# Kernel tuning notes

Measured on AMD Instinct MI355X. Metric: run time of the kernel, lower is better.

Reference implementation:

```python
import jax, jax.numpy as jnp
import numpy as np

N = 256        # SSM state size
D_MODEL = 2048 # number of independent channels sharing the kernel
L_MAX = 4096   # sequence length


def setup_inputs() -> dict:
    key = jax.random.key(0)
    k1, k2, k3, k4 = jax.random.split(key, 4)
    s = float(np.sqrt(N))
    # Stable A: eigenvalues with negative real part so A^l stays bounded after
    # bilinear discretization with step = 1/L.
    A = 0.5 * jax.random.normal(k1, (N, N), jnp.float32) / s - jnp.eye(N, dtype=jnp.float32)
    B = jax.random.normal(k2, (N, 1), jnp.float32) / s   # lecun-scale
    C = jax.random.normal(k3, (1, N), jnp.float32) / s
    D = jnp.ones((1,), jnp.float32)
    y = jax.random.normal(k4, (D_MODEL, L_MAX), jnp.float32)
    return {"y": y, "A": A, "B": B, "C": C, "D": D}


def _build_kernel(A, B, C, L, step):
    # Bilinear (Tustin) discretization, as in discretize_SSM.
    I = jnp.eye(A.shape[0], dtype=A.dtype)
    BL = jnp.linalg.inv(I - (step / 2.0) * A)
    Abar = BL @ (I + (step / 2.0) * A)
    Bbar = (BL * step) @ B                      # (N, 1)
    # K[l] = C @ Abar^l @ Bbar, computed as L matvecs via scan
    # (same math as the matrix_power loop, without O(L*N^3) cost).
    def step_fn(x, _):
        return Abar @ x, (C @ x)[0]
    _, K = jax.lax.scan(step_fn, Bbar[:, 0], None, length=L)
    return K                                     # (L,)


def _causal_conv(y, K):
    # mode='full' convolution truncated to first L samples == causal conv.
    L = y.shape[-1]
    n = 2 * L
    Yf = jnp.fft.rfft(y, n=n, axis=-1)           # (d_model, n//2+1)
    Kf = jnp.fft.rfft(K, n=n)                    # (n//2+1,)
    return jnp.fft.irfft(Yf * Kf, n=n, axis=-1)[..., :L]


def reference(y, A, B, C, D):
    L = y.shape[-1]
    K = _build_kernel(A, B, C, L, step=1.0 / L)
    return _causal_conv(y, K) + D * y
```

## Files before the change

kernel.cpp:

```cpp
#include <hip/hip_runtime.h>

#define N_ 256
#define L_ 4096
#define DM_ 2048
#define STEPF (1.0f / 4096.0f)
#define NW 15
#define NV 6
#define RQN 4608

typedef short bf16x8 __attribute__((ext_vector_type(8)));
typedef float f32x4 __attribute__((ext_vector_type(4)));
typedef unsigned int uint32;

__device__ __forceinline__ uint32 bf16rne(float f) {
    uint32 u = __builtin_bit_cast(uint32, f);
    return (u + 0x7FFFu + ((u >> 16) & 1u)) >> 16;
}
__device__ __forceinline__ float rdlane(float v, int l) {
    return __builtin_bit_cast(float, __builtin_amdgcn_readlane(__builtin_bit_cast(int, v), l));
}

__global__ __launch_bounds__(1024) void k_kry(const float* __restrict__ Araw,
                                              const float* __restrict__ Bv,
                                              const float* __restrict__ Cv,
                                              float* __restrict__ W,
                                              float* __restrict__ V) {
    __shared__ float kry[NW][256];
    __shared__ float red[4][256];
    __shared__ float cur[256];
    const int tid = threadIdx.x;
    const int j = tid & 255, seg = tid >> 8, lane = tid & 63;

#define DOT64(S0, S1, VV) { \
    _Pragma("unroll") \
    for (int m = 0; m < 64; m += 2) { \
        S0 = fmaf(rdlane(VV, m), a[m], S0); \
        S1 = fmaf(rdlane(VV, m + 1), a[m + 1], S1); \
    } }

    if (blockIdx.x == 0) {
        float a[64];
#pragma unroll
        for (int m = 0; m < 64; ++m) a[m] = Araw[(64 * seg + m) * 256 + j];
        if (tid < 256) kry[0][tid] = Cv[tid];
        __syncthreads();
        const float WSC = 4032.0f / 4096.0f;
        for (int n = 1; n < NW; ++n) {
            float vv = kry[n - 1][64 * seg + lane];
            float s0 = 0.f, s1 = 0.f;
            DOT64(s0, s1, vv)
            red[seg][j] = s0 + s1;
            __syncthreads();
            if (tid < 256)
                kry[n][tid] = (red[0][tid] + red[1][tid] + red[2][tid] + red[3][tid]) * (WSC / (float)n);
            __syncthreads();
        }
        float kj[NW];
#pragma unroll
        for (int n = 0; n < NW; ++n) kj[n] = kry[n][j];
        for (int u = 0; u < 16; ++u) {
            int q = seg + 4 * u;
            float c = (float)q * (1.0f / 63.0f);
            float h = kj[NW - 1];
#pragma unroll
            for (int n = NW - 2; n >= 0; --n) h = fmaf(c, h, kj[n]);
            W[q * 256 + j] = h;
        }
    } else {
        float a[64];
#pragma unroll
        for (int m = 0; m < 64; ++m) a[m] = Araw[j * 256 + 64 * seg + m];
        if (tid < 256) cur[tid] = Bv[tid];
        __syncthreads();
        const float ms = 0.5f * STEPF;
        for (int it = 0; it < 3; ++it) {
            float vv = cur[64 * seg + lane];
            float s0 = 0.f, s1 = 0.f;
            DOT64(s0, s1, vv)
            red[seg][j] = s0 + s1;
            __syncthreads();
            if (tid < 256)
                cur[tid] = fmaf(ms, red[0][tid] + red[1][tid] + red[2][tid] + red[3][tid], Bv[tid]);
            __syncthreads();
        }
        if (tid < 256) kry[0][tid] = STEPF * cur[tid];
        __syncthreads();
        const float VSC = 63.0f / 4096.0f;
        for (int n = 1; n < NV; ++n) {
            float vv = kry[n - 1][64 * seg + lane];
            float s0 = 0.f, s1 = 0.f;
            DOT64(s0, s1, vv)
            red[seg][j] = s0 + s1;
            __syncthreads();
            if (tid < 256)
                kry[n][tid] = (red[0][tid] + red[1][tid] + red[2][tid] + red[3][tid]) * (VSC / (float)n);
            __syncthreads();
        }
        float kj[NV];
#pragma unroll
        for (int n = 0; n < NV; ++n) kj[n] = kry[n][j];
        for (int u = 0; u < 16; ++u) {
            int r = seg + 4 * u;
            float c = (float)r * (1.0f / 63.0f);
            float h = kj[NV - 1];
#pragma unroll
            for (int n = NV - 2; n >= 0; --n) h = fmaf(c, h, kj[n]);
            V[j * 64 + r] = h;
        }
    }
#undef DOT64
}

__global__ __launch_bounds__(256) void k_g(const float* __restrict__ A, const float* __restrict__ B,
                                           float* __restrict__ C, int Ma, int Nb,
                                           int lda, int ldb, int ldc, float alpha, float diagv) {
    int row0 = blockIdx.y * 32, col0 = blockIdx.x * 32;
    if (row0 >= Ma || col0 >= Nb) return;
    __shared__ float As[16][33], Bs[16][33];
    int tid = threadIdx.x;
    int tx = tid & 15, ty = tid >> 4;
    int e0 = tid * 2, e1 = e0 + 1;
    int ai0 = e0 >> 4, ak0 = e0 & 15, ai1 = e1 >> 4, ak1 = e1 & 15;
    int bj0 = e0 & 31, bk0 = e0 >> 5, bj1 = e1 & 31, bk1 = e1 >> 5;
    bool va0 = (row0 + ai0) < Ma, va1 = (row0 + ai1) < Ma;
    bool vb0 = (col0 + bj0) < Nb, vb1 = (col0 + bj1) < Nb;
    float a0p = va0 ? A[(row0 + ai0) * lda + ak0] : 0.f;
    float a1p = va1 ? A[(row0 + ai1) * lda + ak1] : 0.f;
    float b0p = vb0 ? B[bk0 * ldb + col0 + bj0] : 0.f;
    float b1p = vb1 ? B[bk1 * ldb + col0 + bj1] : 0.f;
    float acc00 = 0.f, acc01 = 0.f, acc10 = 0.f, acc11 = 0.f;
    for (int kk = 0; kk < 256; kk += 16) {
        As[ak0][ai0] = a0p; As[ak1][ai1] = a1p;
        Bs[bk0][bj0] = b0p; Bs[bk1][bj1] = b1p;
        __syncthreads();
        if (kk + 16 < 256) {
            a0p = va0 ? A[(row0 + ai0) * lda + kk + 16 + ak0] : 0.f;
            a1p = va1 ? A[(row0 + ai1) * lda + kk + 16 + ak1] : 0.f;
            b0p = vb0 ? B[(bk0 + kk + 16) * ldb + col0 + bj0] : 0.f;
            b1p = vb1 ? B[(bk1 + kk + 16) * ldb + col0 + bj1] : 0.f;
        }
#pragma unroll
        for (int k = 0; k < 16; ++k) {
            float a0 = As[k][ty * 2], a1 = As[k][ty * 2 + 1];
            float b0 = Bs[k][tx * 2], b1 = Bs[k][tx * 2 + 1];
            acc00 = fmaf(a0, b0, acc00); acc01 = fmaf(a0, b1, acc01);
            acc10 = fmaf(a1, b0, acc10); acc11 = fmaf(a1, b1, acc11);
        }
        __syncthreads();
    }
    float accs[2][2] = {{acc00, acc01}, {acc10, acc11}};
#pragma unroll
    for (int i = 0; i < 2; ++i) {
        int r = row0 + ty * 2 + i;
        if (r < Ma)
#pragma unroll
            for (int jj = 0; jj < 2; ++jj) {
                int c = col0 + tx * 2 + jj;
                if (c < Nb) {
                    float v = alpha * accs[i][jj];
                    if (r == c) v += diagv;
                    C[r * ldc + c] = v;
                }
            }
    }
}

__global__ __launch_bounds__(256) void k_pack(const float* __restrict__ Kf, uint2* __restrict__ Rqg) {
    int i = blockIdx.x * 256 + threadIdx.x;
    int a = 4095 - i;
    uint32 e0 = (a >= 0) ? bf16rne(Kf[a]) : 0u;
    uint32 e1 = (a >= 1) ? bf16rne(Kf[a - 1]) : 0u;
    uint32 e2 = (a >= 2) ? bf16rne(Kf[a - 2]) : 0u;
    uint32 e3 = (a >= 3) ? bf16rne(Kf[a - 3]) : 0u;
    uint2 v; v.x = e0 | (e1 << 16); v.y = e2 | (e3 << 16);
    Rqg[i] = v;
}

__global__ __launch_bounds__(256, 2) void k_conv(const uint2* __restrict__ Rqg,
                                                 const float* __restrict__ y,
                                                 const float* __restrict__ Dp,
                                                 float* __restrict__ out) {
    __shared__ uint2 Rq[RQN];
    __shared__ f32x4 mbuf[2][8][64];
    const int tid = threadIdx.x;
#pragma unroll
    for (int i = 0; i < RQN / 256; ++i) Rq[i * 256 + tid] = Rqg[i * 256 + tid];
    __syncthreads();

    const int w = tid >> 6, lane = tid & 63;
    const int n = lane & 15, g = lane >> 4;
    const int ds = w & 1, jh = w >> 1;
    const int by = (int)blockIdx.y;
    const int d0w = (int)blockIdx.x * 32 + ds * 16;
    const int d = d0w + n;
    const float4* __restrict__ yq = (const float4*)(y + (size_t)d * L_);
    const float D0 = Dp[0];

#define LOADF(SL, I0) { \
    uint2 u0 = Rq[(I0)]; uint2 u1 = Rq[(I0) + 4]; \
    uint4 uu; uu.x = u0.x; uu.y = u0.y; uu.z = u1.x; uu.w = u1.y; \
    fr[SL] = __builtin_bit_cast(bf16x8, uu); }
#define PK2(LO, HI) __builtin_amdgcn_perm(__builtin_bit_cast(uint32, (HI)), \
                                          __builtin_bit_cast(uint32, (LO)), 0x07060302u)
#define PACKAV(Q0, Q1) { \
    uint4 ua; ua.x = PK2((Q0).x, (Q0).y); ua.y = PK2((Q0).z, (Q0).w); \
    ua.z = PK2((Q1).x, (Q1).y); ua.w = PK2((Q1).z, (Q1).w); \
    av = __builtin_bit_cast(bf16x8, ua); }
#define MF(TI, SL) acc[TI] = __builtin_amdgcn_mfma_f32_16x16x32_bf16(av, fr[SL], acc[TI], 0, 0, 0);

#define STEPB(YI, S0,S1,S2,S3,S4,S5,S6,S7,S8,S9,S10,S11,S12,S13,S14,S15) { \
    PACKAV(q0a, q0b); \
    q0a = q1a; q0b = q1b; \
    __builtin_amdgcn_s_setprio(1); \
    MF(14, S14) MF(15, S15) \
    LOADF(S14, bcur + 32) LOADF(S15, bcur + 16) \
    q1a = yq[(YI)]; q1b = yq[(YI) + 1]; \
    yn += 8; bcur += 32; \
    MF(0,S0) MF(1,S1) MF(2,S2) MF(3,S3) MF(4,S4) MF(5,S5) MF(6,S6) MF(7,S7) \
    MF(8,S8) MF(9,S9) MF(10,S10) MF(11,S11) MF(12,S12) MF(13,S13) \
    __builtin_amdgcn_s_setprio(0); \
}

#define ROUND8(YIM) \
    STEPB(YIM, 0,1,2,3,4,5,6,7,8,9,10,11,12,13,14,15) \
    STEPB(YIM, 14,15,0,1,2,3,4,5,6,7,8,9,10,11,12,13) \
    STEPB(YIM, 12,13,14,15,0,1,2,3,4,5,6,7,8,9,10,11) \
    STEPB(YIM, 10,11,12,13,14,15,0,1,2,3,4,5,6,7,8,9) \
    STEPB(YIM, 8,9,10,11,12,13,14,15,0,1,2,3,4,5,6,7) \
    STEPB(YIM, 6,7,8,9,10,11,12,13,14,15,0,1,2,3,4,5) \
    STEPB(YIM, 4,5,6,7,8,9,10,11,12,13,14,15,0,1,2,3) \
    STEPB(YIM, 2,3,4,5,6,7,8,9,10,11,12,13,14,15,0,1)

#define ROUND4(YIM) \
    STEPB(YIM, 0,1,2,3,4,5,6,7,8,9,10,11,12,13,14,15) \
    STEPB(YIM, 14,15,0,1,2,3,4,5,6,7,8,9,10,11,12,13) \
    STEPB(YIM, 12,13,14,15,0,1,2,3,4,5,6,7,8,9,10,11) \
    STEPB(YIM, 10,11,12,13,14,15,0,1,2,3,4,5,6,7,8,9)

    for (int strip = 0; strip < 2; ++strip) {
        const int v = strip ? by : (15 - by);
        const int t0 = v << 8;
        const int Sh = 4 * (v + 1);
        const int s0 = jh * Sh;

        f32x4 acc[16];
#pragma unroll
        for (int i = 0; i < 16; ++i) acc[i] = (f32x4){0.f, 0.f, 0.f, 0.f};
        bf16x8 fr[16], av;
        float4 q0a, q0b, q1a, q1b;

        const int B0 = 4095 - t0 - n + 8 * g + 32 * s0;
#pragma unroll
        for (int ti = 0; ti < 16; ++ti) LOADF(ti, B0 - 16 * ti)
        q0a = yq[8 * s0 + 2 * g];     q0b = yq[8 * s0 + 2 * g + 1];
        q1a = yq[8 * s0 + 8 + 2 * g]; q1b = yq[8 * s0 + 8 + 2 * g + 1];
        int bcur = B0;
        int yn = 8 * s0 + 16 + 2 * g;

        const int n8 = Sh >> 3;
        for (int it = 0; it < n8 - 1; ++it) {
            ROUND8(yn)
        }
        if (n8 > 0) {
            ROUND8(yn < 1016 ? yn : 1016)
        }
        if (Sh & 4) {
            ROUND4(yn)
        }

#pragma unroll
        for (int rr = 0; rr < 2; ++rr) {
            if (jh == 1) {
#pragma unroll
                for (int i = 0; i < 8; ++i) mbuf[ds][i][lane] = acc[rr * 8 + i];
            }
            __syncthreads();
            if (jh == 0) {
#pragma unroll
                for (int i = 0; i < 8; ++i) {
                    f32x4 m = mbuf[ds][i][lane];
                    acc[rr * 8 + i][0] += m[0]; acc[rr * 8 + i][1] += m[1];
                    acc[rr * 8 + i][2] += m[2]; acc[rr * 8 + i][3] += m[3];
                }
            }
            __syncthreads();
        }
        if (jh == 0) {
#pragma unroll
            for (int ti = 0; ti < 16; ++ti) {
                int tcol = t0 + 16 * ti + n;
#pragma unroll
                for (int r = 0; r < 4; ++r) {
                    int dr = d0w + 4 * g + r;
                    size_t ix = (size_t)dr * L_ + tcol;
                    out[ix] = acc[ti][r] + D0 * y[ix];
                }
            }
        }
    }

#undef ROUND8
#undef ROUND4
#undef STEPB
#undef MF
#undef PACKAV
#undef PK2
#undef LOADF
}


extern "C" void kernel_launch(void* const* d_in, const int* in_sizes, int n_in,
                              void* d_out, int out_size, void* d_ws, size_t ws_size,
                              hipStream_t stream) {
    const float* y  = (const float*)d_in[0];
    const float* A  = (const float*)d_in[1];
    const float* Bv = (const float*)d_in[2];
    const float* Cv = (const float*)d_in[3];
    const float* Dp = (const float*)d_in[4];
    float* out = (float*)d_out;
    float* w = (float*)d_ws;

    float* W   = w;
    float* V   = w + 16384;
    float* Kf  = w + 32768;
    uint2* Rqg = (uint2*)(w + 36864);

    k_kry<<<dim3(2), dim3(1024), 0, stream>>>(A, Bv, Cv, W, V);
    k_g<<<dim3(2, 2), dim3(256), 0, stream>>>(W, V, Kf, 64, 64, 256, 64, 64, 1.0f, 0.0f);
    k_pack<<<dim3(18), dim3(256), 0, stream>>>(Kf, Rqg);
    k_conv<<<dim3(64, 8), dim3(256), 0, stream>>>(Rqg, y, Dp, out);

    (void)in_sizes; (void)n_in; (void)out_size; (void)ws_size;
}
```

Before: 80.27 us.

## Fuse Krylov build, small GEMM and bf16 pack into one kernel

Merges the two-block Krylov kernel, the 64x64 GEMM kernel and the bf16 pack kernel into a single one-block kernel that keeps W, V and Kf in shared memory. This removes two kernel launches and the global round trips for the intermediates. In exchange, the W and V Krylov chains that previously ran in parallel on two blocks now run serially in one block, and about 148KB of shared memory is used.

```diff
diff --git a/kernel.cpp b/kernel.cpp
--- a/kernel.cpp
+++ b/kernel.cpp
@@ -20,16 +20,21 @@
     return __builtin_bit_cast(float, __builtin_amdgcn_readlane(__builtin_bit_cast(int, v), l));
 }
 
-__global__ __launch_bounds__(1024) void k_kry(const float* __restrict__ Araw,
-                                              const float* __restrict__ Bv,
-                                              const float* __restrict__ Cv,
-                                              float* __restrict__ W,
-                                              float* __restrict__ V) {
-    __shared__ float kry[NW][256];
-    __shared__ float red[4][256];
-    __shared__ float cur[256];
+__global__ __launch_bounds__(1024) void k_build(const float* __restrict__ Araw,
+                                                const float* __restrict__ Bv,
+                                                const float* __restrict__ Cv,
+                                                uint2* __restrict__ Rqg) {
+    __shared__ float sm[37888];
+    float* kry = sm;
+    float* red = sm + 3840;
+    float* cur = sm + 4864;
+    float* Wl  = sm + 5120;
+    float* Vl  = sm + 21504;
+    float* Kf  = sm;
+
     const int tid = threadIdx.x;
     const int j = tid & 255, seg = tid >> 8, lane = tid & 63;
+    float a[64];
 
 #define DOT64(S0, S1, VV) { \
     _Pragma("unroll") \
@@ -38,142 +43,116 @@
         S1 = fmaf(rdlane(VV, m + 1), a[m + 1], S1); \
     } }
 
-    if (blockIdx.x == 0) {
-        float a[64];
-#pragma unroll
-        for (int m = 0; m < 64; ++m) a[m] = Araw[(64 * seg + m) * 256 + j];
-        if (tid < 256) kry[0][tid] = Cv[tid];
-        __syncthreads();
-        const float WSC = 4032.0f / 4096.0f;
-        for (int n = 1; n < NW; ++n) {
-            float vv = kry[n - 1][64 * seg + lane];
-            float s0 = 0.f, s1 = 0.f;
-            DOT64(s0, s1, vv)
-            red[seg][j] = s0 + s1;
-            __syncthreads();
-            if (tid < 256)
-                kry[n][tid] = (red[0][tid] + red[1][tid] + red[2][tid] + red[3][tid]) * (WSC / (float)n);
-            __syncthreads();
-        }
+#pragma unroll
+    for (int m = 0; m < 64; ++m) a[m] = Araw[(64 * seg + m) * 256 + j];
+    if (tid < 256) kry[0 * 256 + tid] = Cv[tid];
+    __syncthreads();
+    const float WSC = 4032.0f / 4096.0f;
+    for (int n = 1; n < NW; ++n) {
+        float vv = kry[(n - 1) * 256 + 64 * seg + lane];
+        float s0 = 0.f, s1 = 0.f;
+        DOT64(s0, s1, vv)
+        red[seg * 256 + j] = s0 + s1;
+        __syncthreads();
+        if (tid < 256)
+            kry[n * 256 + tid] = (red[tid] + red[256 + tid] + red[512 + tid] + red[768 + tid]) * (WSC / (float)n);
+        __syncthreads();
+    }
+    {
         float kj[NW];
 #pragma unroll
-        for (int n = 0; n < NW; ++n) kj[n] = kry[n][j];
+        for (int n = 0; n < NW; ++n) kj[n] = kry[n * 256 + j];
+#pragma unroll
         for (int u = 0; u < 16; ++u) {
             int q = seg + 4 * u;
             float c = (float)q * (1.0f / 63.0f);
             float h = kj[NW - 1];
 #pragma unroll
             for (int n = NW - 2; n >= 0; --n) h = fmaf(c, h, kj[n]);
-            W[q * 256 + j] = h;
-        }
-    } else {
-        float a[64];
-#pragma unroll
-        for (int m = 0; m < 64; ++m) a[m] = Araw[j * 256 + 64 * seg + m];
-        if (tid < 256) cur[tid] = Bv[tid];
-        __syncthreads();
-        const float ms = 0.5f * STEPF;
-        for (int it = 0; it < 3; ++it) {
-            float vv = cur[64 * seg + lane];
-            float s0 = 0.f, s1 = 0.f;
-            DOT64(s0, s1, vv)
-            red[seg][j] = s0 + s1;
-            __syncthreads();
-            if (tid < 256)
-                cur[tid] = fmaf(ms, red[0][tid] + red[1][tid] + red[2][tid] + red[3][tid], Bv[tid]);
-            __syncthreads();
-        }
-        if (tid < 256) kry[0][tid] = STEPF * cur[tid];
-        __syncthreads();
-        const float VSC = 63.0f / 4096.0f;
-        for (int n = 1; n < NV; ++n) {
-            float vv = kry[n - 1][64 * seg + lane];
-            float s0 = 0.f, s1 = 0.f;
-            DOT64(s0, s1, vv)
-            red[seg][j] = s0 + s1;
-            __syncthreads();
-            if (tid < 256)
-                kry[n][tid] = (red[0][tid] + red[1][tid] + red[2][tid] + red[3][tid]) * (VSC / (float)n);
-            __syncthreads();
-        }
+            Wl[q * 256 + j] = h;
+        }
+    }
+
+    {
+        const float4* Ar = (const float4*)(Araw + (size_t)j * 256 + 64 * seg);
+#pragma unroll
+        for (int m4 = 0; m4 < 16; ++m4) {
+            float4 q4 = Ar[m4];
+            a[4 * m4] = q4.x; a[4 * m4 + 1] = q4.y; a[4 * m4 + 2] = q4.z; a[4 * m4 + 3] = q4.w;
+        }
+    }
+    if (tid < 256) cur[tid] = Bv[tid];
+    __syncthreads();
+    const float ms = 0.5f * STEPF;
+    for (int it = 0; it < 3; ++it) {
+        float vv = cur[64 * seg + lane];
+        float s0 = 0.f, s1 = 0.f;
+        DOT64(s0, s1, vv)
+        red[seg * 256 + j] = s0 + s1;
+        __syncthreads();
+        if (tid < 256)
+            cur[tid] = fmaf(ms, red[tid] + red[256 + tid] + red[512 + tid] + red[768 + tid], Bv[tid]);
+        __syncthreads();
+    }
+    if (tid < 256) kry[0 * 256 + tid] = STEPF * cur[tid];
+    __syncthreads();
+    const float VSC = 63.0f / 4096.0f;
+    for (int n = 1; n < NV; ++n) {
+        float vv = kry[(n - 1) * 256 + 64 * seg + lane];
+        float s0 = 0.f, s1 = 0.f;
+        DOT64(s0, s1, vv)
+        red[seg * 256 + j] = s0 + s1;
+        __syncthreads();
+        if (tid < 256)
+            kry[n * 256 + tid] = (red[tid] + red[256 + tid] + red[512 + tid] + red[768 + tid]) * (VSC / (float)n);
+        __syncthreads();
+    }
+    {
         float kj[NV];
 #pragma unroll
-        for (int n = 0; n < NV; ++n) kj[n] = kry[n][j];
+        for (int n = 0; n < NV; ++n) kj[n] = kry[n * 256 + j];
+#pragma unroll
         for (int u = 0; u < 16; ++u) {
             int r = seg + 4 * u;
             float c = (float)r * (1.0f / 63.0f);
             float h = kj[NV - 1];
 #pragma unroll
             for (int n = NV - 2; n >= 0; --n) h = fmaf(c, h, kj[n]);
-            V[j * 64 + r] = h;
-        }
+            Vl[j * 64 + r] = h;
+        }
+    }
+    __syncthreads();
+
+    {
+        const int q = tid >> 4, rb = (tid & 15) * 4;
+        f32x4 acc = (f32x4){0.f, 0.f, 0.f, 0.f};
+        for (int k = 0; k < 256; k += 4) {
+            float4 wq = *(const float4*)&Wl[q * 256 + k];
+#pragma unroll
+            for (int kk = 0; kk < 4; ++kk) {
+                float wv = ((const float*)&wq)[kk];
+                float4 v4 = *(const float4*)&Vl[(k + kk) * 64 + rb];
+                acc[0] = fmaf(wv, v4.x, acc[0]); acc[1] = fmaf(wv, v4.y, acc[1]);
+                acc[2] = fmaf(wv, v4.z, acc[2]); acc[3] = fmaf(wv, v4.w, acc[3]);
+            }
+        }
+        Kf[q * 64 + rb]     = acc[0];
+        Kf[q * 64 + rb + 1] = acc[1];
+        Kf[q * 64 + rb + 2] = acc[2];
+        Kf[q * 64 + rb + 3] = acc[3];
+    }
+    __syncthreads();
+
+    for (int i = tid; i < RQN; i += 1024) {
+        int aa = 4095 - i;
+        uint32 e0 = (aa >= 0) ? bf16rne(Kf[aa]) : 0u;
+        uint32 e1 = (aa >= 1) ? bf16rne(Kf[aa - 1]) : 0u;
+        uint32 e2 = (aa >= 2) ? bf16rne(Kf[aa - 2]) : 0u;
+        uint32 e3 = (aa >= 3) ? bf16rne(Kf[aa - 3]) : 0u;
+        uint2 v; v.x = e0 | (e1 << 16); v.y = e2 | (e3 << 16);
+        Rqg[i] = v;
     }
 #undef DOT64
-}
-
-__global__ __launch_bounds__(256) void k_g(const float* __restrict__ A, const float* __restrict__ B,
-                                           float* __restrict__ C, int Ma, int Nb,
-                                           int lda, int ldb, int ldc, float alpha, float diagv) {
-    int row0 = blockIdx.y * 32, col0 = blockIdx.x * 32;
-    if (row0 >= Ma || col0 >= Nb) return;
-    __shared__ float As[16][33], Bs[16][33];
-    int tid = threadIdx.x;
-    int tx = tid & 15, ty = tid >> 4;
-    int e0 = tid * 2, e1 = e0 + 1;
-    int ai0 = e0 >> 4, ak0 = e0 & 15, ai1 = e1 >> 4, ak1 = e1 & 15;
-    int bj0 = e0 & 31, bk0 = e0 >> 5, bj1 = e1 & 31, bk1 = e1 >> 5;
-    bool va0 = (row0 + ai0) < Ma, va1 = (row0 + ai1) < Ma;
-    bool vb0 = (col0 + bj0) < Nb, vb1 = (col0 + bj1) < Nb;
-    float a0p = va0 ? A[(row0 + ai0) * lda + ak0] : 0.f;
-    float a1p = va1 ? A[(row0 + ai1) * lda + ak1] : 0.f;
-    float b0p = vb0 ? B[bk0 * ldb + col0 + bj0] : 0.f;
-    float b1p = vb1 ? B[bk1 * ldb + col0 + bj1] : 0.f;
-    float acc00 = 0.f, acc01 = 0.f, acc10 = 0.f, acc11 = 0.f;
-    for (int kk = 0; kk < 256; kk += 16) {
-        As[ak0][ai0] = a0p; As[ak1][ai1] = a1p;
-        Bs[bk0][bj0] = b0p; Bs[bk1][bj1] = b1p;
-        __syncthreads();
-        if (kk + 16 < 256) {
-            a0p = va0 ? A[(row0 + ai0) * lda + kk + 16 + ak0] : 0.f;
-            a1p = va1 ? A[(row0 + ai1) * lda + kk + 16 + ak1] : 0.f;
-            b0p = vb0 ? B[(bk0 + kk + 16) * ldb + col0 + bj0] : 0.f;
-            b1p = vb1 ? B[(bk1 + kk + 16) * ldb + col0 + bj1] : 0.f;
-        }
-#pragma unroll
-        for (int k = 0; k < 16; ++k) {
-            float a0 = As[k][ty * 2], a1 = As[k][ty * 2 + 1];
-            float b0 = Bs[k][tx * 2], b1 = Bs[k][tx * 2 + 1];
-            acc00 = fmaf(a0, b0, acc00); acc01 = fmaf(a0, b1, acc01);
-            acc10 = fmaf(a1, b0, acc10); acc11 = fmaf(a1, b1, acc11);
-        }
-        __syncthreads();
-    }
-    float accs[2][2] = {{acc00, acc01}, {acc10, acc11}};
-#pragma unroll
-    for (int i = 0; i < 2; ++i) {
-        int r = row0 + ty * 2 + i;
-        if (r < Ma)
-#pragma unroll
-            for (int jj = 0; jj < 2; ++jj) {
-                int c = col0 + tx * 2 + jj;
-                if (c < Nb) {
-                    float v = alpha * accs[i][jj];
-                    if (r == c) v += diagv;
-                    C[r * ldc + c] = v;
-                }
-            }
-    }
-}
-
-__global__ __launch_bounds__(256) void k_pack(const float* __restrict__ Kf, uint2* __restrict__ Rqg) {
-    int i = blockIdx.x * 256 + threadIdx.x;
-    int a = 4095 - i;
-    uint32 e0 = (a >= 0) ? bf16rne(Kf[a]) : 0u;
-    uint32 e1 = (a >= 1) ? bf16rne(Kf[a - 1]) : 0u;
-    uint32 e2 = (a >= 2) ? bf16rne(Kf[a - 2]) : 0u;
-    uint32 e3 = (a >= 3) ? bf16rne(Kf[a - 3]) : 0u;
-    uint2 v; v.x = e0 | (e1 << 16); v.y = e2 | (e3 << 16);
-    Rqg[i] = v;
 }
 
 __global__ __launch_bounds__(256, 2) void k_conv(const uint2* __restrict__ Rqg,
@@ -318,16 +297,9 @@
     const float* Cv = (const float*)d_in[3];
     const float* Dp = (const float*)d_in[4];
     float* out = (float*)d_out;
-    float* w = (float*)d_ws;
-
-    float* W   = w;
-    float* V   = w + 16384;
-    float* Kf  = w + 32768;
-    uint2* Rqg = (uint2*)(w + 36864);
-
-    k_kry<<<dim3(2), dim3(1024), 0, stream>>>(A, Bv, Cv, W, V);
-    k_g<<<dim3(2, 2), dim3(256), 0, stream>>>(W, V, Kf, 64, 64, 256, 64, 64, 1.0f, 0.0f);
-    k_pack<<<dim3(18), dim3(256), 0, stream>>>(Kf, Rqg);
+    uint2* Rqg = (uint2*)d_ws;
+
+    k_build<<<dim3(1), dim3(1024), 0, stream>>>(A, Bv, Cv, Rqg);
     k_conv<<<dim3(64, 8), dim3(256), 0, stream>>>(Rqg, y, Dp, out);
 
     (void)in_sizes; (void)n_in; (void)out_size; (void)ws_size;
```

Result: slower. 93.74 us (+16.8%).
